# Kernel tuning notes

Hardware: AMD Instinct MI355X
Metric: run time of the kernel (lower is better)

## Reference

```python
import jax, jax.numpy as jnp
import numpy as np

B, S, E = 4, 2048, 512
H = 8
DK = E // H          # 64
NQ = 8               # n_qubits


def setup_inputs() -> dict:
    key = jax.random.key(0)
    ks = jax.random.split(key, 10)
    s = 1.0 / np.sqrt(E)
    return {
        "x": jax.random.normal(ks[0], (B, S, E), dtype=jnp.float32),
        "Wq": jax.random.normal(ks[1], (E, E), dtype=jnp.float32) * s,
        "bq": jnp.zeros((E,), dtype=jnp.float32),
        "Wk": jax.random.normal(ks[2], (E, E), dtype=jnp.float32) * s,
        "bk": jnp.zeros((E,), dtype=jnp.float32),
        "Wv": jax.random.normal(ks[3], (E, E), dtype=jnp.float32) * s,
        "bv": jnp.zeros((E,), dtype=jnp.float32),
        "Wo": jax.random.normal(ks[4], (E, E), dtype=jnp.float32) * s,
        "bo": jnp.zeros((E,), dtype=jnp.float32),
        "kernel_params": jax.random.normal(ks[5], (NQ, NQ), dtype=jnp.float32),
    }


def _split_heads(t):
    # [B,S,E] -> [B,H,S,DK]
    return t.reshape(B, S, H, DK).transpose(0, 2, 1, 3)


def reference(x, Wq, bq, Wk, bk, Wv, bv, Wo, bo, kernel_params):
    q = _split_heads(x @ Wq + bq)
    k = _split_heads(x @ Wk + bk)
    v = _split_heads(x @ Wv + bv)

    # Quantum kernel closed form: RX(x_i) then RZ(theta_ii) on wire i, measure <Z_i>.
    # RZ commutes with Z so <Z_i> = cos(x_i). Only the first NQ features are encoded.
    q_meas = jnp.cos(q[..., :NQ])  # [B,H,S,NQ]
    k_meas = jnp.cos(k[..., :NQ])  # [B,H,S,NQ]

    sim = jnp.einsum('bhqd,bhkd->bhqk', q_meas, k_meas)  # [B,H,S,S]
    attn = jax.nn.softmax(sim, axis=-1)
    out = jnp.einsum('bhqk,bhkd->bhqd', attn, v)          # [B,H,S,DK]
    out = out.transpose(0, 2, 1, 3).reshape(B, S, E)      # compose heads
    return out @ Wo + bo
```

## Files before the change

### kernel.cpp

```cpp
#include <hip/hip_runtime.h>
#include <hip/hip_bf16.h>

#define BB 4
#define SS 2048
#define EE 512
#define HH 8
#define DKK 64
#define NQQ 8
#define BS (BB * SS)

typedef __attribute__((ext_vector_type(8))) short bf16x8;
typedef __attribute__((ext_vector_type(4))) float f32x4;
typedef __attribute__((ext_vector_type(16))) float f32x16;
typedef _Float16 f16x4 __attribute__((ext_vector_type(4)));
typedef _Float16 f16x8 __attribute__((ext_vector_type(8)));
typedef unsigned short u16;
typedef unsigned int u32;

union U2H { uint2 u; f16x4 h; };
union U4H8 { uint4 u; f16x8 h; };

__device__ __forceinline__ u16 f2bf(float f) {
    union { float f; u32 u; } v; v.f = f;
    u32 r = v.u + 0x7fffu + ((v.u >> 16) & 1u);
    return (u16)(r >> 16);
}
__device__ __forceinline__ float bf2f(u16 h) {
    union { u32 u; float f; } v; v.u = ((u32)h) << 16;
    return v.f;
}
__device__ __forceinline__ u16 f2h(float f) {
    _Float16 hv = (_Float16)f;
    return *reinterpret_cast<u16*>(&hv);
}

__global__ __launch_bounds__(256) void cvt2_kernel(
    const float4* __restrict__ in, uint2* __restrict__ xh, uint2* __restrict__ xl, int n4)
{
    int i = blockIdx.x * 256 + threadIdx.x;
    if (i >= n4) return;
    float4 a = in[i];
    u16 h0 = f2bf(a.x), h1 = f2bf(a.y), h2 = f2bf(a.z), h3 = f2bf(a.w);
    u16 l0 = f2bf(a.x - bf2f(h0)), l1 = f2bf(a.y - bf2f(h1));
    u16 l2 = f2bf(a.z - bf2f(h2)), l3 = f2bf(a.w - bf2f(h3));
    xh[i] = make_uint2((u32)h0 | ((u32)h1 << 16), (u32)h2 | ((u32)h3 << 16));
    xl[i] = make_uint2((u32)l0 | ((u32)l1 << 16), (u32)l2 | ((u32)l3 << 16));
}

__global__ __launch_bounds__(256) void wqk_pack_kernel(
    const float* __restrict__ Wq, const float* __restrict__ Wk,
    u16* __restrict__ Wh, u16* __restrict__ Wl)
{
    const int n = blockIdx.x;
    const int col = (((n & 63) >> 3) << 6) | (n & 7);
    const float* src = (n < 64) ? Wq : Wk;
    for (int k = threadIdx.x; k < EE; k += 256) {
        float v = src[(size_t)k * EE + col];
        u16 h = f2bf(v);
        Wh[(size_t)n * EE + k] = h;
        Wl[(size_t)n * EE + k] = f2bf(v - bf2f(h));
    }
}

__global__ __launch_bounds__(256) void wtrans_kernel(
    const float* __restrict__ W, u16* __restrict__ WT)
{
    __shared__ float ts[64][65];
    const int kt0 = blockIdx.x * 64, nt0 = blockIdx.y * 64;
    const int tid = threadIdx.x;
    #pragma unroll
    for (int i = 0; i < 4; ++i) {
        int c = tid + i * 256;
        int kr = c >> 4, nc = (c & 15) * 4;
        float4 t = *reinterpret_cast<const float4*>(&W[(size_t)(kt0 + kr) * EE + nt0 + nc]);
        ts[kr][nc] = t.x; ts[kr][nc + 1] = t.y; ts[kr][nc + 2] = t.z; ts[kr][nc + 3] = t.w;
    }
    __syncthreads();
    const int n = tid >> 2, k0 = (tid & 3) * 16;
    u32 o[8];
    #pragma unroll
    for (int j = 0; j < 8; ++j) {
        o[j] = (u32)f2bf(ts[k0 + 2 * j][n]) | ((u32)f2bf(ts[k0 + 2 * j + 1][n]) << 16);
    }
    uint4* dst = reinterpret_cast<uint4*>(&WT[(size_t)(nt0 + n) * EE + kt0 + k0]);
    dst[0] = make_uint4(o[0], o[1], o[2], o[3]);
    dst[1] = make_uint4(o[4], o[5], o[6], o[7]);
}

__global__ __launch_bounds__(256) void qk_mfma_kernel(
    const u16* __restrict__ xh, const u16* __restrict__ xl,
    const u16* __restrict__ Wh, const u16* __restrict__ Wl,
    const float* __restrict__ bq, const float* __restrict__ bk,
    u16* __restrict__ qf, u16* __restrict__ kf)
{
    __shared__ u16 Asl[64 * 64];
    __shared__ u16 Bsl[64 * 64];

    const int tid = threadIdx.x;
    const int lane = tid & 63;
    const int ww = tid >> 6;
    const int wr = ww >> 1, wc = ww & 1;
    const int tx = lane & 15, tyq = lane >> 4;
    const int m0 = blockIdx.x * 64;
    const int isK = blockIdx.y;
    const int nbase = isK * 64;

    const int c0 = tid, c1 = tid + 256;
    const int r0 = c0 >> 3, o0 = (c0 & 7) * 8, d0 = r0 * 64 + (((c0 & 7) ^ (r0 & 7)) * 8);
    const int r1 = c1 >> 3, o1 = (c1 & 7) * 8, d1 = r1 * 64 + (((c1 & 7) ^ (r1 & 7)) * 8);

    uint4 pa0, pa1, pb0, pb1;
    auto ldi = [&](int it) {
        int pass = it >> 3, k0 = (it & 7) * 64;
        const u16* Ab = (pass == 1) ? xl : xh;
        const u16* Bb = (pass == 2) ? Wl : Wh;
        pa0 = *reinterpret_cast<const uint4*>(&Ab[(size_t)(m0 + r0) * EE + k0 + o0]);
        pb0 = *reinterpret_cast<const uint4*>(&Bb[(size_t)(nbase + r0) * EE + k0 + o0]);
        pa1 = *reinterpret_cast<const uint4*>(&Ab[(size_t)(m0 + r1) * EE + k0 + o1]);
        pb1 = *reinterpret_cast<const uint4*>(&Bb[(size_t)(nbase + r1) * EE + k0 + o1]);
    };
    auto st = [&]() {
        *reinterpret_cast<uint4*>(&Asl[d0]) = pa0;
        *reinterpret_cast<uint4*>(&Bsl[d0]) = pb0;
        *reinterpret_cast<uint4*>(&Asl[d1]) = pa1;
        *reinterpret_cast<uint4*>(&Bsl[d1]) = pb1;
    };

    f32x4 acc[2][2];
    #pragma unroll
    for (int mt = 0; mt < 2; ++mt)
        #pragma unroll
        for (int nt = 0; nt < 2; ++nt) acc[mt][nt] = (f32x4)(0.f);

    const int bkx = tx & 7;
    ldi(0);
    for (int it = 0; it < 24; ++it) {
        __syncthreads();
        st();
        if (it < 23) ldi(it + 1);
        __syncthreads();
        #pragma unroll
        for (int kb = 0; kb < 2; ++kb) {
            bf16x8 af[2], bfg[2];
            const int kblk = ((kb * 4 + tyq) ^ bkx) * 8;
            #pragma unroll
            for (int mt = 0; mt < 2; ++mt)
                af[mt] = *reinterpret_cast<const bf16x8*>(&Asl[(wr * 32 + mt * 16 + tx) * 64 + kblk]);
            #pragma unroll
            for (int nt = 0; nt < 2; ++nt)
                bfg[nt] = *reinterpret_cast<const bf16x8*>(&Bsl[(wc * 32 + nt * 16 + tx) * 64 + kblk]);
            #pragma unroll
            for (int mt = 0; mt < 2; ++mt)
                #pragma unroll
                for (int nt = 0; nt < 2; ++nt)
                    acc[mt][nt] = __builtin_amdgcn_mfma_f32_16x16x32_bf16(
                        af[mt], bfg[nt], acc[mt][nt], 0, 0, 0);
        }
    }

    const float* bias = isK ? bk : bq;
    u16* dst = isK ? kf : qf;
    #pragma unroll
    for (int mt = 0; mt < 2; ++mt) {
        #pragma unroll
        for (int nt = 0; nt < 2; ++nt) {
            int nl = wc * 32 + nt * 16 + tx;
            int h = nl >> 3, f = nl & 7;
            float bcol = bias[h * 64 + f];
            #pragma unroll
            for (int r = 0; r < 4; ++r) {
                int s = m0 + wr * 32 + mt * 16 + tyq * 4 + r;
                float c = __cosf(acc[mt][nt][r] + bcol);
                size_t bh = (size_t)((s >> 11) * HH + h);
                dst[(bh * SS + (s & 2047)) * 8 + f] = f2h(c);
            }
        }
    }
}

template<int MODE>
__global__ __launch_bounds__(256) void mfma_gemm_kernel(
    const u16* __restrict__ A, const u16* __restrict__ Bm,
    const float* __restrict__ bias, float* __restrict__ outf, u16* __restrict__ outb)
{
    __shared__ u16 Asl[64 * 64];
    __shared__ u16 Bsl[64 * 64];

    const int tid = threadIdx.x;
    const int lane = tid & 63;
    const int ww = tid >> 6;
    const int wr = ww >> 1, wc = ww & 1;
    const int tx = lane & 15, tyq = lane >> 4;
    const int m0 = blockIdx.x * 64, n0 = blockIdx.y * 64;

    const int c0 = tid, c1 = tid + 256;
    const int r0 = c0 >> 3, o0 = (c0 & 7) * 8, d0 = r0 * 64 + (((c0 & 7) ^ (r0 & 7)) * 8);
    const int r1 = c1 >> 3, o1 = (c1 & 7) * 8, d1 = r1 * 64 + (((c1 & 7) ^ (r1 & 7)) * 8);

    uint4 pa0, pa1, pb0, pb1;
    auto ld = [&](int ks) {
        int k0 = ks * 64;
        pa0 = *reinterpret_cast<const uint4*>(&A [(size_t)(m0 + r0) * EE + k0 + o0]);
        pb0 = *reinterpret_cast<const uint4*>(&Bm[(size_t)(n0 + r0) * EE + k0 + o0]);
        pa1 = *reinterpret_cast<const uint4*>(&A [(size_t)(m0 + r1) * EE + k0 + o1]);
        pb1 = *reinterpret_cast<const uint4*>(&Bm[(size_t)(n0 + r1) * EE + k0 + o1]);
    };
    auto st = [&]() {
        *reinterpret_cast<uint4*>(&Asl[d0]) = pa0;
        *reinterpret_cast<uint4*>(&Bsl[d0]) = pb0;
        *reinterpret_cast<uint4*>(&Asl[d1]) = pa1;
        *reinterpret_cast<uint4*>(&Bsl[d1]) = pb1;
    };

    f32x4 acc[2][2];
    #pragma unroll
    for (int mt = 0; mt < 2; ++mt)
        #pragma unroll
        for (int nt = 0; nt < 2; ++nt) acc[mt][nt] = (f32x4)(0.f);

    const int bkx = tx & 7;
    ld(0);
    for (int ks = 0; ks < 8; ++ks) {
        __syncthreads();
        st();
        if (ks < 7) ld(ks + 1);
        __syncthreads();
        #pragma unroll
        for (int kb = 0; kb < 2; ++kb) {
            bf16x8 af[2], bfg[2];
            const int kblk = ((kb * 4 + tyq) ^ bkx) * 8;
            #pragma unroll
            for (int mt = 0; mt < 2; ++mt)
                af[mt] = *reinterpret_cast<const bf16x8*>(&Asl[(wr * 32 + mt * 16 + tx) * 64 + kblk]);
            #pragma unroll
            for (int nt = 0; nt < 2; ++nt)
                bfg[nt] = *reinterpret_cast<const bf16x8*>(&Bsl[(wc * 32 + nt * 16 + tx) * 64 + kblk]);
            #pragma unroll
            for (int mt = 0; mt < 2; ++mt)
                #pragma unroll
                for (int nt = 0; nt < 2; ++nt)
                    acc[mt][nt] = __builtin_amdgcn_mfma_f32_16x16x32_bf16(
                        af[mt], bfg[nt], acc[mt][nt], 0, 0, 0);
        }
    }

    #pragma unroll
    for (int mt = 0; mt < 2; ++mt) {
        #pragma unroll
        for (int nt = 0; nt < 2; ++nt) {
            int gcol = n0 + wc * 32 + nt * 16 + tx;
            float bcol = (MODE == 0) ? bias[gcol] : 0.f;
            #pragma unroll
            for (int r = 0; r < 4; ++r) {
                int grow = m0 + wr * 32 + mt * 16 + tyq * 4 + r;
                float v = acc[mt][nt][r];
                if (MODE == 0) {
                    outf[(size_t)grow * EE + gcol] = v + bcol;
                } else {
                    float vb = v + bias[grow];
                    size_t addr = ((size_t)((gcol >> 11) * 8 + (grow >> 6))) * (64 * 2048)
                                + (size_t)(grow & 63) * 2048 + (gcol & 2047);
                    outb[addr] = f2h(vb);
                }
            }
        }
    }
}

__global__ __launch_bounds__(256) void attn_v5_kernel(
    const u16* __restrict__ qf, const u16* __restrict__ kf,
    const u16* __restrict__ VT, u16* __restrict__ attb)
{
    __shared__ u16 vtl[64 * 64];

    const int tid = threadIdx.x;
    const int lane = tid & 63;
    const int wq = tid >> 6;
    const int l31 = lane & 31;
    const int hi = lane >> 5;

    const int bid = blockIdx.x;
    const int xcd = bid & 7, sub = bid >> 3;
    const int bh = (xcd << 2) | (sub >> 4);
    const int q0 = (sub & 15) * 128;

    const u16* __restrict__ qfb = qf + (size_t)bh * SS * 8;
    const u16* __restrict__ kfb = kf + (size_t)bh * SS * 8;
    const u16* __restrict__ VTb = VT + (size_t)bh * DKK * SS;

    const uint4 z4 = make_uint4(0u, 0u, 0u, 0u);

    U4H8 qb;
    qb.u = hi ? z4 : *reinterpret_cast<const uint4*>(&qfb[(size_t)(q0 + wq * 32 + l31) * 8]);
    const f16x8 QB = qb.h;

    const int wd0 = tid >> 3, wbk = tid & 7;
    const int B0 = (wbk >> 1) * 2;
    const int offu = (wbk & 1) * 4;
    const int w0a = wd0 * 64 + ((B0 ^ (wd0 & 7)) * 8) + offu;
    const int w0b = wd0 * 64 + (((B0 + 1) ^ (wd0 & 7)) * 8) + offu;
    const int wd1 = wd0 + 32;
    const int w1a = wd1 * 64 + ((B0 ^ (wd1 & 7)) * 8) + offu;
    const int w1b = wd1 * 64 + (((B0 + 1) ^ (wd1 & 7)) * 8) + offu;

    uint4 pv0, pv1;
    auto ldv = [&](int kt) {
        pv0 = *reinterpret_cast<const uint4*>(&VTb[(size_t)wd0 * SS + kt + wbk * 8]);
        pv1 = *reinterpret_cast<const uint4*>(&VTb[(size_t)wd1 * SS + kt + wbk * 8]);
    };
    auto stv = [&]() {
        *reinterpret_cast<uint2*>(&vtl[w0a]) = make_uint2(pv0.x, pv0.y);
        *reinterpret_cast<uint2*>(&vtl[w0b]) = make_uint2(pv0.z, pv0.w);
        *reinterpret_cast<uint2*>(&vtl[w1a]) = make_uint2(pv1.x, pv1.y);
        *reinterpret_cast<uint2*>(&vtl[w1b]) = make_uint2(pv1.z, pv1.w);
    };

    f32x16 acc0 = (f32x16)(0.f);
    f32x16 acc1 = (f32x16)(0.f);
    float z = 0.f;

    const int vr0 = l31 * 64;
    const int vr1 = (32 + l31) * 64;
    const int bx = l31 & 7;

    ldv(0);
    for (int kt = 0; kt < SS; kt += 64) {
        __syncthreads();
        stv();
        if (kt + 64 < SS) ldv(kt + 64);
        __syncthreads();

        U4H8 ka0, ka1;
        ka0.u = hi ? z4 : *reinterpret_cast<const uint4*>(&kfb[(size_t)(kt + l31) * 8]);
        ka1.u = hi ? z4 : *reinterpret_cast<const uint4*>(&kfb[(size_t)(kt + 32 + l31) * 8]);

        #pragma unroll
        for (int s = 0; s < 2; ++s) {
            f32x16 sim = (f32x16)(0.f);
            sim = __builtin_amdgcn_mfma_f32_32x32x16_f16(
                s ? ka1.h : ka0.h, QB, sim, 0, 0, 0);

            float w[16];
            #pragma unroll
            for (int r = 0; r < 16; ++r) w[r] = __expf(sim[r]);
            float zp = 0.f;
            #pragma unroll
            for (int r = 0; r < 8; ++r) zp += (w[2 * r] + w[2 * r + 1]);
            z += zp;

            #pragma unroll
            for (int c = 0; c < 2; ++c) {
                f16x8 PA;
                #pragma unroll
                for (int j = 0; j < 8; ++j) PA[j] = (_Float16)w[8 * c + j];
                const int e = s * 4 + c * 2;
                f16x8 VB0 = *reinterpret_cast<const f16x8*>(&vtl[vr0 + (((e + hi) ^ bx) * 8)]);
                acc0 = __builtin_amdgcn_mfma_f32_32x32x16_f16(PA, VB0, acc0, 0, 0, 0);
                f16x8 VB1 = *reinterpret_cast<const f16x8*>(&vtl[vr1 + (((e + hi) ^ bx) * 8)]);
                acc1 = __builtin_amdgcn_mfma_f32_32x32x16_f16(PA, VB1, acc1, 0, 0, 0);
            }
        }
    }

    z += __shfl_xor(z, 32, 64);
    float zinv = 1.0f / z;

    const int b = bh >> 3, h = bh & 7;
    #pragma unroll
    for (int r = 0; r < 16; ++r) {
        int qrow = (r & 3) + 8 * (r >> 2) + 4 * hi;
        float zi = __shfl(zinv, qrow, 32);
        size_t base = ((size_t)b * SS + q0 + wq * 32 + qrow) * EE + h * DKK + l31;
        attb[base]      = f2bf(acc0[r] * zi);
        attb[base + 32] = f2bf(acc1[r] * zi);
    }
}

extern "C" void kernel_launch(void* const* d_in, const int* in_sizes, int n_in,
                              void* d_out, int out_size, void* d_ws, size_t ws_size,
                              hipStream_t stream)
{
    const float* x  = (const float*)d_in[0];
    const float* Wq = (const float*)d_in[1];
    const float* bq = (const float*)d_in[2];
    const float* Wk = (const float*)d_in[3];
    const float* bk = (const float*)d_in[4];
    const float* Wv = (const float*)d_in[5];
    const float* bv = (const float*)d_in[6];
    const float* Wo = (const float*)d_in[7];
    const float* bo = (const float*)d_in[8];

    char* w = (char*)d_ws;
    u16* xh    = (u16*)w;  w += (size_t)BS * EE * 2;
    u16* xl    = (u16*)w;  w += (size_t)BS * EE * 2;
    u16* Wqkh  = (u16*)w;  w += (size_t)128 * EE * 2;
    u16* Wqkl  = (u16*)w;  w += (size_t)128 * EE * 2;
    u16* WvT   = (u16*)w;  w += (size_t)EE * EE * 2;
    u16* WoT   = (u16*)w;  w += (size_t)EE * EE * 2;
    u16* qf    = (u16*)w;  w += (size_t)BB * HH * SS * 8 * 2;
    u16* kf    = (u16*)w;  w += (size_t)BB * HH * SS * 8 * 2;
    u16* VT    = (u16*)w;  w += (size_t)BB * HH * DKK * SS * 2;
    u16* attb  = xl;
    float* out = (float*)d_out;

    cvt2_kernel<<<dim3(BS * EE / 4 / 256), 256, 0, stream>>>(
        (const float4*)x, (uint2*)xh, (uint2*)xl, BS * EE / 4);
    wqk_pack_kernel<<<dim3(128), 256, 0, stream>>>(Wq, Wk, Wqkh, Wqkl);
    wtrans_kernel<<<dim3(8, 8), 256, 0, stream>>>(Wv, WvT);
    wtrans_kernel<<<dim3(8, 8), 256, 0, stream>>>(Wo, WoT);
    qk_mfma_kernel<<<dim3(BS / 64, 2), 256, 0, stream>>>(
        xh, xl, Wqkh, Wqkl, bq, bk, qf, kf);
    mfma_gemm_kernel<1><<<dim3(EE / 64, BS / 64), 256, 0, stream>>>(
        WvT, xh, bv, nullptr, VT);
    attn_v5_kernel<<<dim3(512), 256, 0, stream>>>(qf, kf, VT, attb);
    mfma_gemm_kernel<0><<<dim3(BS / 64, EE / 64), 256, 0, stream>>>(
        attb, WoT, bo, out, nullptr);
}
```

Before: 97.45 us.

## Split attention key range across waves with double-buffered V tiles and LDS reduction

The attention kernel now gives each block 64 queries instead of 128 and splits the key dimension between two wave pairs, which doubles the grid to 1024 blocks. V tiles for both key halves are double-buffered in shared memory, so each iteration needs one barrier instead of two, and K fragments are prefetched one tile ahead. The two partial accumulators and normalizers are combined through shared memory at the end. This raises parallelism and overlaps loads with compute, at the cost of more LDS per block and an extra reduction step.

After: 89.97 us. 1.08x faster.

```diff
diff --git a/kernel.cpp b/kernel.cpp
--- a/kernel.cpp
+++ b/kernel.cpp
@@ -267,22 +267,24 @@
     }
 }
 
-__global__ __launch_bounds__(256) void attn_v5_kernel(
+__global__ __launch_bounds__(256, 4) void attn_v6_kernel(
     const u16* __restrict__ qf, const u16* __restrict__ kf,
     const u16* __restrict__ VT, u16* __restrict__ attb)
 {
-    __shared__ u16 vtl[64 * 64];
+    __shared__ u16 vtl[2][2][64 * 64];
 
     const int tid = threadIdx.x;
     const int lane = tid & 63;
-    const int wq = tid >> 6;
+    const int wv = tid >> 6;
+    const int kslice = wv >> 1;
+    const int qw = wv & 1;
     const int l31 = lane & 31;
     const int hi = lane >> 5;
 
     const int bid = blockIdx.x;
     const int xcd = bid & 7, sub = bid >> 3;
-    const int bh = (xcd << 2) | (sub >> 4);
-    const int q0 = (sub & 15) * 128;
+    const int bh = (xcd << 2) | (sub >> 5);
+    const int q0 = (sub & 31) * 64;
 
     const u16* __restrict__ qfb = qf + (size_t)bh * SS * 8;
     const u16* __restrict__ kfb = kf + (size_t)bh * SS * 8;
@@ -291,7 +293,7 @@
     const uint4 z4 = make_uint4(0u, 0u, 0u, 0u);
 
     U4H8 qb;
-    qb.u = hi ? z4 : *reinterpret_cast<const uint4*>(&qfb[(size_t)(q0 + wq * 32 + l31) * 8]);
+    qb.u = hi ? z4 : *reinterpret_cast<const uint4*>(&qfb[(size_t)(q0 + qw * 32 + l31) * 8]);
     const f16x8 QB = qb.h;
 
     const int wd0 = tid >> 3, wbk = tid & 7;
@@ -303,42 +305,55 @@
     const int w1a = wd1 * 64 + ((B0 ^ (wd1 & 7)) * 8) + offu;
     const int w1b = wd1 * 64 + (((B0 + 1) ^ (wd1 & 7)) * 8) + offu;
 
-    uint4 pv0, pv1;
-    auto ldv = [&](int kt) {
-        pv0 = *reinterpret_cast<const uint4*>(&VTb[(size_t)wd0 * SS + kt + wbk * 8]);
-        pv1 = *reinterpret_cast<const uint4*>(&VTb[(size_t)wd1 * SS + kt + wbk * 8]);
-    };
-    auto stv = [&]() {
-        *reinterpret_cast<uint2*>(&vtl[w0a]) = make_uint2(pv0.x, pv0.y);
-        *reinterpret_cast<uint2*>(&vtl[w0b]) = make_uint2(pv0.z, pv0.w);
-        *reinterpret_cast<uint2*>(&vtl[w1a]) = make_uint2(pv1.x, pv1.y);
-        *reinterpret_cast<uint2*>(&vtl[w1b]) = make_uint2(pv1.z, pv1.w);
-    };
-
-    f32x16 acc0 = (f32x16)(0.f);
-    f32x16 acc1 = (f32x16)(0.f);
+    uint4 pv[2][2];
+    auto ldv = [&](int t) {
+        #pragma unroll
+        for (int s = 0; s < 2; ++s) {
+            int kt = s * 1024 + t * 64;
+            pv[s][0] = *reinterpret_cast<const uint4*>(&VTb[(size_t)wd0 * SS + kt + wbk * 8]);
+            pv[s][1] = *reinterpret_cast<const uint4*>(&VTb[(size_t)wd1 * SS + kt + wbk * 8]);
+        }
+    };
+    auto stv = [&](int buf) {
+        #pragma unroll
+        for (int s = 0; s < 2; ++s) {
+            u16* base = &vtl[s][buf][0];
+            *reinterpret_cast<uint2*>(&base[w0a]) = make_uint2(pv[s][0].x, pv[s][0].y);
+            *reinterpret_cast<uint2*>(&base[w0b]) = make_uint2(pv[s][0].z, pv[s][0].w);
+            *reinterpret_cast<uint2*>(&base[w1a]) = make_uint2(pv[s][1].x, pv[s][1].y);
+            *reinterpret_cast<uint2*>(&base[w1b]) = make_uint2(pv[s][1].z, pv[s][1].w);
+        }
+    };
+
+    f32x16 acc0 = (f32x16)(0.f), acc1 = (f32x16)(0.f);
     float z = 0.f;
 
-    const int vr0 = l31 * 64;
-    const int vr1 = (32 + l31) * 64;
+    const int vr0 = l31 * 64, vr1 = (32 + l31) * 64;
     const int bx = l31 & 7;
+    const int ks_off = kslice * 1024;
+
+    U4H8 kc0, kc1, kn0, kn1;
+    auto ldk = [&](int t, U4H8& a, U4H8& b) {
+        int kt = ks_off + t * 64;
+        a.u = hi ? z4 : *reinterpret_cast<const uint4*>(&kfb[(size_t)(kt + l31) * 8]);
+        b.u = hi ? z4 : *reinterpret_cast<const uint4*>(&kfb[(size_t)(kt + 32 + l31) * 8]);
+    };
 
     ldv(0);
-    for (int kt = 0; kt < SS; kt += 64) {
-        __syncthreads();
-        stv();
-        if (kt + 64 < SS) ldv(kt + 64);
-        __syncthreads();
-
-        U4H8 ka0, ka1;
-        ka0.u = hi ? z4 : *reinterpret_cast<const uint4*>(&kfb[(size_t)(kt + l31) * 8]);
-        ka1.u = hi ? z4 : *reinterpret_cast<const uint4*>(&kfb[(size_t)(kt + 32 + l31) * 8]);
-
+    ldk(0, kc0, kc1);
+    stv(0);
+    __syncthreads();
+
+    for (int t = 0; t < 16; ++t) {
+        const int cur = t & 1;
+        if (t < 15) { ldv(t + 1); ldk(t + 1, kn0, kn1); }
+
+        const u16* vbase = &vtl[kslice][cur][0];
         #pragma unroll
         for (int s = 0; s < 2; ++s) {
             f32x16 sim = (f32x16)(0.f);
             sim = __builtin_amdgcn_mfma_f32_32x32x16_f16(
-                s ? ka1.h : ka0.h, QB, sim, 0, 0, 0);
+                s ? kc1.h : kc0.h, QB, sim, 0, 0, 0);
 
             float w[16];
             #pragma unroll
@@ -354,25 +369,48 @@
                 #pragma unroll
                 for (int j = 0; j < 8; ++j) PA[j] = (_Float16)w[8 * c + j];
                 const int e = s * 4 + c * 2;
-                f16x8 VB0 = *reinterpret_cast<const f16x8*>(&vtl[vr0 + (((e + hi) ^ bx) * 8)]);
+                f16x8 VB0 = *reinterpret_cast<const f16x8*>(&vbase[vr0 + (((e + hi) ^ bx) * 8)]);
                 acc0 = __builtin_amdgcn_mfma_f32_32x32x16_f16(PA, VB0, acc0, 0, 0, 0);
-                f16x8 VB1 = *reinterpret_cast<const f16x8*>(&vtl[vr1 + (((e + hi) ^ bx) * 8)]);
+                f16x8 VB1 = *reinterpret_cast<const f16x8*>(&vbase[vr1 + (((e + hi) ^ bx) * 8)]);
                 acc1 = __builtin_amdgcn_mfma_f32_32x32x16_f16(PA, VB1, acc1, 0, 0, 0);
             }
         }
-    }
-
-    z += __shfl_xor(z, 32, 64);
-    float zinv = 1.0f / z;
-
-    const int b = bh >> 3, h = bh & 7;
-    #pragma unroll
-    for (int r = 0; r < 16; ++r) {
-        int qrow = (r & 3) + 8 * (r >> 2) + 4 * hi;
-        float zi = __shfl(zinv, qrow, 32);
-        size_t base = ((size_t)b * SS + q0 + wq * 32 + qrow) * EE + h * DKK + l31;
-        attb[base]      = f2bf(acc0[r] * zi);
-        attb[base + 32] = f2bf(acc1[r] * zi);
+
+        if (t < 15) stv(cur ^ 1);
+        __syncthreads();
+        kc0 = kn0; kc1 = kn1;
+    }
+
+    float* fsh = reinterpret_cast<float*>(&vtl[0][0][0]);
+    const int cbase = (qw * 64 + lane) * 33;
+    if (kslice == 1) {
+        #pragma unroll
+        for (int r = 0; r < 16; ++r) {
+            fsh[cbase + r] = acc0[r];
+            fsh[cbase + 16 + r] = acc1[r];
+        }
+        fsh[cbase + 32] = z;
+    }
+    __syncthreads();
+    if (kslice == 0) {
+        #pragma unroll
+        for (int r = 0; r < 16; ++r) {
+            acc0[r] += fsh[cbase + r];
+            acc1[r] += fsh[cbase + 16 + r];
+        }
+        z += fsh[cbase + 32];
+        z += __shfl_xor(z, 32, 64);
+        float zinv = 1.0f / z;
+
+        const int b = bh >> 3, h = bh & 7;
+        #pragma unroll
+        for (int r = 0; r < 16; ++r) {
+            int qrow = (r & 3) + 8 * (r >> 2) + 4 * hi;
+            float zi = __shfl(zinv, qrow, 32);
+            size_t base = ((size_t)b * SS + q0 + qw * 32 + qrow) * EE + h * DKK + l31;
+            attb[base]      = f2bf(acc0[r] * zi);
+            attb[base + 32] = f2bf(acc1[r] * zi);
+        }
     }
 }
 
@@ -412,7 +450,7 @@
         xh, xl, Wqkh, Wqkl, bq, bk, qf, kf);
     mfma_gemm_kernel<1><<<dim3(EE / 64, BS / 64), 256, 0, stream>>>(
         WvT, xh, bv, nullptr, VT);
-    attn_v5_kernel<<<dim3(512), 256, 0, stream>>>(qf, kf, VT, attb);
+    attn_v6_kernel<<<dim3(1024), 256, 0, stream>>>(qf, kf, VT, attb);
     mfma_gemm_kernel<0><<<dim3(BS / 64, EE / 64), 256, 0, stream>>>(
         attb, WoT, bo, out, nullptr);
 }
```
